# Kernel optimization log

Hardware: AMD Instinct MI355X
Metric: run time of the kernel (lower is better)

The kernel has to match this reference:

```python
import jax, jax.numpy as jnp
import numpy as np

C, CH, H = 128, 32, 4  # c_in, c_hidden, n_head


def _layer_norm(x, w, b, eps=1e-5):
    mu = jnp.mean(x, axis=-1, keepdims=True)
    var = jnp.var(x, axis=-1, keepdims=True)
    return (x - mu) * jax.lax.rsqrt(var + eps) * w + b


def _tri_attn(x, ln_w, ln_b, wq, wk, wv, wz, wg, bg, wo, bo):
    # x: [B, I, J, C]; attention runs over J independently for each row I
    B, I, J, _ = x.shape
    x = _layer_norm(x, ln_w, ln_b)
    q = (x @ wq).reshape(B, I, J, H, CH) * (CH ** -0.5)
    k = (x @ wk).reshape(B, I, J, H, CH)
    v = (x @ wv).reshape(B, I, J, H, CH)
    # learned pairwise triangle bias: [B, I, J, H] -> [B, 1, H, I, J]
    tb = jnp.transpose(x @ wz, (0, 3, 1, 2))[:, None]
    scores = jnp.einsum('biqhd,bikhd->bihqk', q, k) + tb  # [B, I, H, J, J]
    a = jax.nn.softmax(scores, axis=-1)
    o = jnp.einsum('bihqk,bikhd->biqhd', a, v)
    g = jax.nn.sigmoid(x @ wg + bg).reshape(B, I, J, H, CH)
    o = (o * g).reshape(B, I, J, H * CH)
    return o @ wo + bo


def setup_inputs() -> dict:
    key = jax.random.key(0)
    ks = jax.random.split(key, 16)
    B, N = 1, 256
    inp = {'cmap': jax.random.normal(ks[0], (B, C, N, N), jnp.float32)}
    for i, p in enumerate(['s', 'e']):
        kq, kk, kv, kz, kg, ko = jax.random.split(ks[1 + i], 6)
        sd = 0.02
        inp[p + '_ln_w'] = jnp.ones((C,), jnp.float32)
        inp[p + '_ln_b'] = jnp.zeros((C,), jnp.float32)
        inp[p + '_wq'] = jax.random.normal(kq, (C, H * CH), jnp.float32) * sd
        inp[p + '_wk'] = jax.random.normal(kk, (C, H * CH), jnp.float32) * sd
        inp[p + '_wv'] = jax.random.normal(kv, (C, H * CH), jnp.float32) * sd
        inp[p + '_wz'] = jax.random.normal(kz, (C, H), jnp.float32) * sd
        inp[p + '_wg'] = jax.random.normal(kg, (C, H * CH), jnp.float32) * sd
        inp[p + '_bg'] = jnp.ones((H * CH,), jnp.float32)  # gating bias init = 1
        inp[p + '_wo'] = jax.random.normal(ko, (H * CH, C), jnp.float32) * sd
        inp[p + '_bo'] = jnp.zeros((C,), jnp.float32)
    return inp


def reference(cmap,
              s_ln_w, s_ln_b, s_wq, s_wk, s_wv, s_wz, s_wg, s_bg, s_wo, s_bo,
              e_ln_w, e_ln_b, e_wq, e_wk, e_wv, e_wz, e_wg, e_bg, e_wo, e_bo):
    # cmap: [B, C, I, J] -> channels last [B, I, J, C]
    x = jnp.transpose(cmap, (0, 2, 3, 1))
    # triangle attention around starting node (dropout is identity in eval)
    x = x + _tri_attn(x, s_ln_w, s_ln_b, s_wq, s_wk, s_wv, s_wz, s_wg, s_bg, s_wo, s_bo)
    # triangle attention around ending node: transpose I<->J, attend, transpose back
    xt = jnp.swapaxes(x, 1, 2)
    x = x + jnp.swapaxes(
        _tri_attn(xt, e_ln_w, e_ln_b, e_wq, e_wk, e_wv, e_wz, e_wg, e_bg, e_wo, e_bo), 1, 2)
    return jnp.transpose(x, (0, 3, 1, 2))
```

## Files before the change

### kernel.cpp

```cpp
#include <hip/hip_runtime.h>
#include <hip/hip_bf16.h>

#define NNX 256
#define CCX 128
#define HHX 4
#define CHDX 32
#define NIJ (NNX*NNX)

typedef __hip_bfloat16 bf16;
typedef __hip_bfloat162 bf162;
typedef __attribute__((ext_vector_type(8))) short short8v;
typedef __attribute__((ext_vector_type(4))) float float4v;
typedef __attribute__((ext_vector_type(4))) unsigned int uint4v;

__device__ __forceinline__ float4v MFMA(short8v a, short8v b, float4v c){
  return __builtin_amdgcn_mfma_f32_16x16x32_bf16(a, b, c, 0, 0, 0);
}

__device__ __forceinline__ unsigned pk2(float a, float b){
  unsigned short ua = __bfloat16_as_ushort(__float2bfloat16(a));
  unsigned short ub = __bfloat16_as_ushort(__float2bfloat16(b));
  return (unsigned)ua | ((unsigned)ub << 16);
}
__device__ __forceinline__ float ubf(unsigned short u){
  return __bfloat162float(__ushort_as_bfloat16(u));
}

__device__ __forceinline__ void load8bf16(const bf16* p, float* f){
  const bf162* p2 = (const bf162*)p;
  #pragma unroll
  for(int t=0;t<4;++t){ float2 xy = __bfloat1622float2(p2[t]); f[2*t]=xy.x; f[2*t+1]=xy.y; }
}

__global__ __launch_bounds__(256) void k_tin(const float* __restrict__ in, float* __restrict__ out){
  __shared__ float t[32][33];
  const int i = blockIdx.z, jt = blockIdx.x, ct = blockIdx.y;
  const int tx = threadIdx.x, ty = threadIdx.y;
  #pragma unroll
  for(int k=0;k<32;k+=8){
    int c = ct*32 + ty + k;
    t[ty+k][tx] = in[(size_t)c*NIJ + (size_t)i*NNX + jt*32 + tx];
  }
  __syncthreads();
  #pragma unroll
  for(int k=0;k<32;k+=8){
    int j = jt*32 + ty + k;
    out[((size_t)i*NNX + j)*CCX + ct*32 + tx] = t[tx][ty+k];
  }
}

__global__ __launch_bounds__(256) void k_tout(const float* __restrict__ x, float* __restrict__ out){
  __shared__ float t[32][33];
  const int i = blockIdx.z, jt = blockIdx.x, ct = blockIdx.y;
  const int tx = threadIdx.x, ty = threadIdx.y;
  #pragma unroll
  for(int k=0;k<32;k+=8){
    t[ty+k][tx] = x[((size_t)i*NNX + jt*32+ty+k)*CCX + ct*32 + tx];
  }
  __syncthreads();
  #pragma unroll
  for(int k=0;k<32;k+=8){
    out[(size_t)(ct*32+ty+k)*NIJ + (size_t)i*NNX + jt*32 + tx] = t[tx][ty+k];
  }
}

template<int TRANS>
__global__ __launch_bounds__(256) void k_lntb(const float* __restrict__ x,
    const float* __restrict__ w, const float* __restrict__ b,
    const float* __restrict__ wz, bf16* __restrict__ xln, float* __restrict__ tb2){
  const int r = blockIdx.x*4 + threadIdx.y;
  const int ii = r>>8, jj = r&255;
  const float* src = x + (size_t)(TRANS ? (jj*NNX+ii) : r)*CCX;
  const int c = threadIdx.x*2;
  float2 v = *(const float2*)(src+c);
  float s = v.x+v.y, s2 = v.x*v.x+v.y*v.y;
  #pragma unroll
  for(int off=32; off>0; off>>=1){ s += __shfl_xor(s,off); s2 += __shfl_xor(s2,off); }
  float mu = s*0.0078125f;
  float var = s2*0.0078125f - mu*mu;
  float rs = rsqrtf(var+1e-5f);
  float a0 = (v.x-mu)*rs*w[c]+b[c];
  float a1 = (v.y-mu)*rs*w[c+1]+b[c+1];
  bf162 hp; hp.x = __float2bfloat16(a0); hp.y = __float2bfloat16(a1);
  *(bf162*)(xln + (size_t)r*CCX + c) = hp;
  float acc[4];
  #pragma unroll
  for(int hh=0;hh<4;++hh) acc[hh] = a0*wz[c*4+hh] + a1*wz[(c+1)*4+hh];
  #pragma unroll
  for(int off=32; off>0; off>>=1){
    #pragma unroll
    for(int hh=0;hh<4;++hh) acc[hh] += __shfl_xor(acc[hh], off);
  }
  if(threadIdx.x==0){
    #pragma unroll
    for(int hh=0;hh<4;++hh) tb2[(size_t)hh*NIJ + r] = acc[hh];
  }
}

__global__ __launch_bounds__(256) void k_cvtw(const float* __restrict__ wq,
    const float* __restrict__ wk, const float* __restrict__ wv,
    const float* __restrict__ wg, const float* __restrict__ wo, bf16* __restrict__ wT){
  int idx = blockIdx.x*256 + threadIdx.x;
  if(idx < 65536){
    int n = idx >> 7, k = idx & 127;
    const float* W = (n<128)?wq:(n<256)?wk:(n<384)?wv:wg;
    wT[idx] = __float2bfloat16(W[k*CCX + (n&127)]);
  } else {
    int idx2 = idx - 65536;
    int n = idx2 >> 7, k = idx2 & 127;
    wT[idx] = __float2bfloat16(wo[k*CCX + n]);
  }
}

template<int SUB>
__device__ __forceinline__ void attn_sub(const int mb,
    const int lq, const int g, const int l,
    short8v qf, uint2 pgl, uint2 pgh,
    char* ksb, const char* vtb, const float* tbq_base, bf16* __restrict__ obh){
  const int q0 = mb + SUB*16;
  const int q  = q0 + lq;
  const float* tbq = tbq_base + (size_t)q*NNX;
  float4v s[16];
  __builtin_amdgcn_s_setprio(1);
  #pragma unroll
  for(int t=0;t<16;++t){
    short8v ak = *(const short8v*)(ksb + (size_t)(t*16 + lq)*80 + g*16);
    float4v bb = *(const float4v*)(tbq + t*16 + g*4);
    s[t] = MFMA(ak, qf, bb);
  }
  __builtin_amdgcn_s_setprio(0);
  float m = -1e30f;
  #pragma unroll
  for(int t=0;t<16;++t)
    m = fmaxf(m, fmaxf(fmaxf(s[t][0], s[t][1]), fmaxf(s[t][2], s[t][3])));
  m = fmaxf(m, __shfl_xor(m,16));
  m = fmaxf(m, __shfl_xor(m,32));
  float lsum = 0.f;
  #pragma unroll
  for(int t=0;t<16;++t){
    #pragma unroll
    for(int r=0;r<4;++r){ float e = __expf(s[t][r]-m); s[t][r]=e; lsum+=e; }
  }
  lsum += __shfl_xor(lsum,16);
  lsum += __shfl_xor(lsum,32);
  const float linv = 1.0f/lsum;
  #pragma unroll
  for(int dt=0; dt<2; ++dt){
    float4v acc = (float4v)(0.f);
    __builtin_amdgcn_s_setprio(1);
    #pragma unroll
    for(int c=0;c<8;++c){
      const int vrow = dt*16 + lq;
      short8v av = *(const short8v*)(vtb + (size_t)vrow*512 + ((16*g + 64*c) ^ ((vrow&7)<<4)));
      uint4 pb;
      pb.x = pk2(s[2*c][0],   s[2*c][1]);
      pb.y = pk2(s[2*c][2],   s[2*c][3]);
      pb.z = pk2(s[2*c+1][0], s[2*c+1][1]);
      pb.w = pk2(s[2*c+1][2], s[2*c+1][3]);
      short8v bp;
      bp[0]=(short)(pb.x&0xffff); bp[1]=(short)(pb.x>>16);
      bp[2]=(short)(pb.y&0xffff); bp[3]=(short)(pb.y>>16);
      bp[4]=(short)(pb.z&0xffff); bp[5]=(short)(pb.z>>16);
      bp[6]=(short)(pb.w&0xffff); bp[7]=(short)(pb.w>>16);
      acc = MFMA(av, bp, acc);
    }
    __builtin_amdgcn_s_setprio(0);
    const uint2 pg = dt ? pgh : pgl;
    float g0 = ubf((unsigned short)(pg.x & 0xffff));
    float g1 = ubf((unsigned short)(pg.x >> 16));
    float g2 = ubf((unsigned short)(pg.y & 0xffff));
    float g3 = ubf((unsigned short)(pg.y >> 16));
    float o0 = acc[0]*linv / (1.f + __expf(-g0));
    float o1 = acc[1]*linv / (1.f + __expf(-g1));
    float o2 = acc[2]*linv / (1.f + __expf(-g2));
    float o3 = acc[3]*linv / (1.f + __expf(-g3));
    uint2 pw; pw.x = pk2(o0,o1); pw.y = pk2(o2,o3);
    *(uint2*)(ksb + (size_t)(mb + lq*4 + 2*dt + (g>>1))*80 + 64 + (g&1)*8) = pw;
  }
  {
    const int r2 = l >> 2, c2 = l & 3;
    uint4v ow = *(const uint4v*)(ksb + (size_t)(mb + r2*4 + c2)*80 + 64);
    __builtin_nontemporal_store(ow, (uint4v*)(obh + (size_t)(q0 + r2)*CHDX + c2*8));
  }
}

__global__ __launch_bounds__(256,4) void k_fattn(const bf16* __restrict__ xln,
    const bf16* __restrict__ wT, const float* __restrict__ bg,
    const float* __restrict__ tb2, bf16* __restrict__ op){
  __shared__ unsigned short Ks[256*40];
  __shared__ unsigned short Vt[32*256];
  const int id = blockIdx.x;
  const int h = id >> 8, i = id & 255;
  const int tid = threadIdx.x;
  const int w = tid >> 6, l = tid & 63;
  const int lq = l & 15, g = l >> 4;
  const int mb = w*64;

  char* ksb = (char*)Ks;
  char* vtb = (char*)Vt;

  short8v bx[4][4];
  #pragma unroll
  for(int ms=0; ms<4; ++ms){
    const size_t row = (size_t)i*NNX + mb + ms*16 + lq;
    #pragma unroll
    for(int kc=0; kc<4; ++kc)
      bx[ms][kc] = *(const short8v*)(xln + row*CCX + kc*32 + g*8);
  }

  uint4v qfr[4];
  uint2 pgl[4], pgh[4];

  {
    uint2 pqa[4][2];
    #pragma unroll
    for(int half=0; half<2; ++half){
      const int n0 = h*32 + half*16;
      float4v acc[4];
      #pragma unroll
      for(int ms=0; ms<4; ++ms) acc[ms] = (float4v)(0.f);
      #pragma unroll
      for(int kc=0; kc<4; ++kc){
        short8v aw = *(const short8v*)(wT + (size_t)(n0 + lq)*CCX + kc*32 + g*8);
        #pragma unroll
        for(int ms=0; ms<4; ++ms) acc[ms] = MFMA(aw, bx[ms][kc], acc[ms]);
      }
      #pragma unroll
      for(int ms=0; ms<4; ++ms){
        pqa[ms][half].x = pk2(acc[ms][0]*0.17677669529663687f, acc[ms][1]*0.17677669529663687f);
        pqa[ms][half].y = pk2(acc[ms][2]*0.17677669529663687f, acc[ms][3]*0.17677669529663687f);
      }
    }
    const int srcA = lq + 32*(g&1);
    const int hsel = g >> 1;
    #pragma unroll
    for(int ms=0; ms<4; ++ms){
      unsigned sx = hsel ? pqa[ms][1].x : pqa[ms][0].x;
      unsigned sy = hsel ? pqa[ms][1].y : pqa[ms][0].y;
      qfr[ms].x = __shfl(sx, srcA);
      qfr[ms].y = __shfl(sy, srcA);
      qfr[ms].z = __shfl(sx, srcA+16);
      qfr[ms].w = __shfl(sy, srcA+16);
    }
  }

  #pragma unroll
  for(int half=0; half<2; ++half){
    const int n0 = 128 + h*32 + half*16;
    float4v acc[4];
    #pragma unroll
    for(int ms=0; ms<4; ++ms) acc[ms] = (float4v)(0.f);
    #pragma unroll
    for(int kc=0; kc<4; ++kc){
      short8v aw = *(const short8v*)(wT + (size_t)(n0 + lq)*CCX + kc*32 + g*8);
      #pragma unroll
      for(int ms=0; ms<4; ++ms) acc[ms] = MFMA(aw, bx[ms][kc], acc[ms]);
    }
    #pragma unroll
    for(int ms=0; ms<4; ++ms){
      const int row = mb + ms*16 + lq;
      uint2 pw; pw.x = pk2(acc[ms][0], acc[ms][1]);
                pw.y = pk2(acc[ms][2], acc[ms][3]);
      *(uint2*)(ksb + (size_t)row*80 + half*32 + g*8) = pw;
    }
  }

  #pragma unroll
  for(int half=0; half<2; ++half){
    const int n0 = 256 + h*32 + half*16;
    float4v acc[4];
    #pragma unroll
    for(int ms=0; ms<4; ++ms) acc[ms] = (float4v)(0.f);
    #pragma unroll
    for(int kc=0; kc<4; ++kc){
      short8v aw = *(const short8v*)(wT + (size_t)(n0 + lq)*CCX + kc*32 + g*8);
      #pragma unroll
      for(int ms=0; ms<4; ++ms) acc[ms] = MFMA(aw, bx[ms][kc], acc[ms]);
    }
    #pragma unroll
    for(int ms=0; ms<4; ++ms){
      const int k = mb + ms*16 + lq;
      const int j = k & 31;
      const int kap = (k & ~31) + 8*((j>>2)&3) + 4*((j>>4)&1) + (j&3);
      #pragma unroll
      for(int r=0; r<4; ++r){
        const int d = half*16 + 4*g + r;
        const int off = d*512 + ((2*kap) ^ ((d&7)<<4));
        *(unsigned short*)(vtb + off) = __bfloat16_as_ushort(__float2bfloat16(acc[ms][r]));
      }
    }
  }

  #pragma unroll
  for(int half=0; half<2; ++half){
    const int n0 = 384 + h*32 + half*16;
    float4v acc[4];
    #pragma unroll
    for(int ms=0; ms<4; ++ms) acc[ms] = (float4v)(0.f);
    #pragma unroll
    for(int kc=0; kc<4; ++kc){
      short8v aw = *(const short8v*)(wT + (size_t)(n0 + lq)*CCX + kc*32 + g*8);
      #pragma unroll
      for(int ms=0; ms<4; ++ms) acc[ms] = MFMA(aw, bx[ms][kc], acc[ms]);
    }
    const float4 bg4 = *(const float4*)(bg + h*32 + half*16 + 4*g);
    #pragma unroll
    for(int ms=0; ms<4; ++ms){
      uint2 pw; pw.x = pk2(acc[ms][0]+bg4.x, acc[ms][1]+bg4.y);
                pw.y = pk2(acc[ms][2]+bg4.z, acc[ms][3]+bg4.w);
      if(half==0) pgl[ms] = pw; else pgh[ms] = pw;
    }
  }
  __syncthreads();

  bf16* obh = op + ((size_t)h*NIJ + (size_t)i*NNX)*CHDX;
  const float* tbq_base = tb2 + (size_t)h*NIJ;
  attn_sub<0>(mb, lq, g, l, __builtin_bit_cast(short8v, qfr[0]), pgl[0], pgh[0], ksb, vtb, tbq_base, obh);
  attn_sub<1>(mb, lq, g, l, __builtin_bit_cast(short8v, qfr[1]), pgl[1], pgh[1], ksb, vtb, tbq_base, obh);
  attn_sub<2>(mb, lq, g, l, __builtin_bit_cast(short8v, qfr[2]), pgl[2], pgh[2], ksb, vtb, tbq_base, obh);
  attn_sub<3>(mb, lq, g, l, __builtin_bit_cast(short8v, qfr[3]), pgl[3], pgh[3], ksb, vtb, tbq_base, obh);
}

template<int TRANS>
__global__ __launch_bounds__(256) void k_oprojm(const bf16* __restrict__ ob,
    const bf16* __restrict__ woT, const float* __restrict__ bo, float* __restrict__ x){
  const int tid = threadIdx.x;
  const int w = tid >> 6, l = tid & 63;
  const int lq = l & 15, g = l >> 4;
  const int mbase = blockIdx.x*128 + w*32;
  short8v bx[2][4];
  #pragma unroll
  for(int ms=0; ms<2; ++ms){
    const size_t mrow = mbase + ms*16 + lq;
    #pragma unroll
    for(int kc=0; kc<4; ++kc)
      bx[ms][kc] = *(const short8v*)(ob + ((size_t)kc*NIJ + mrow)*CHDX + g*8);
  }
  #pragma unroll
  for(int nj=0; nj<8; ++nj){
    float4v acc0 = (float4v)(0.f), acc1 = (float4v)(0.f);
    #pragma unroll
    for(int kc=0; kc<4; ++kc){
      short8v aw = *(const short8v*)(woT + (size_t)(nj*16 + lq)*CCX + kc*32 + g*8);
      acc0 = MFMA(aw, bx[0][kc], acc0);
      acc1 = MFMA(aw, bx[1][kc], acc1);
    }
    const int col = nj*16 + 4*g;
    const float4 bo4 = *(const float4*)(bo + col);
    #pragma unroll
    for(int ms=0; ms<2; ++ms){
      const int r = mbase + ms*16 + lq;
      const int ii = r>>8, jj = r&255;
      float* dst = x + (size_t)(TRANS ? (jj*NNX+ii) : r)*CCX + col;
      float4 xv = *(float4*)dst;
      xv.x += ((ms==0)?acc0[0]:acc1[0]) + bo4.x;
      xv.y += ((ms==0)?acc0[1]:acc1[1]) + bo4.y;
      xv.z += ((ms==0)?acc0[2]:acc1[2]) + bo4.z;
      xv.w += ((ms==0)?acc0[3]:acc1[3]) + bo4.w;
      *(float4*)dst = xv;
    }
  }
}

extern "C" void kernel_launch(void* const* d_in, const int* in_sizes, int n_in,
                              void* d_out, int out_size, void* d_ws, size_t ws_size,
                              hipStream_t stream){
  const float* cmap = (const float*)d_in[0];
  char* ws = (char*)d_ws;
  float* x   = (float*)(ws);
  bf16* xln  = (bf16*)(ws + 33554432);
  bf16* ob   = (bf16*)(ws + 50331648);
  float* tb2 = (float*)(ws + 117440512);
  bf16* wT   = (bf16*)d_out;
  bf16* woT  = wT + 65536;
  float* outp = (float*)d_out;

  k_tin<<<dim3(8,4,NNX), dim3(32,8), 0, stream>>>(cmap, x);

  for(int p=0;p<2;++p){
    const int b = 1 + 10*p;
    const float* lnw = (const float*)d_in[b+0];
    const float* lnb = (const float*)d_in[b+1];
    const float* wq  = (const float*)d_in[b+2];
    const float* wk  = (const float*)d_in[b+3];
    const float* wv  = (const float*)d_in[b+4];
    const float* wz  = (const float*)d_in[b+5];
    const float* wg  = (const float*)d_in[b+6];
    const float* bg  = (const float*)d_in[b+7];
    const float* wo  = (const float*)d_in[b+8];
    const float* bo  = (const float*)d_in[b+9];

    k_cvtw<<<320, 256, 0, stream>>>(wq, wk, wv, wg, wo, wT);

    if(p==0) k_lntb<0><<<NIJ/4, dim3(64,4), 0, stream>>>(x, lnw, lnb, wz, xln, tb2);
    else     k_lntb<1><<<NIJ/4, dim3(64,4), 0, stream>>>(x, lnw, lnb, wz, xln, tb2);

    k_fattn<<<1024, 256, 0, stream>>>(xln, wT, bg, tb2, ob);

    if(p==0) k_oprojm<0><<<NIJ/128, 256, 0, stream>>>(ob, woT, bo, x);
    else     k_oprojm<1><<<NIJ/128, 256, 0, stream>>>(ob, woT, bo, x);
  }

  k_tout<<<dim3(8,4,NNX), dim3(32,8), 0, stream>>>(x, outp);
}
```

Measured before the change: 250.3 us.

## Fuse input transpose with first layernorm; stage Q in LDS instead of shuffles

Replaces the separate channels-last transpose kernel with a fused kernel that transposes cmap through shared memory and, in the same pass, computes layernorm, the bf16 normalized activations and the triangle bias for the first attention. This drops one full read and write of the activation tensor. In the attention kernel, Q is now written to a new LDS buffer and reloaded per sub-tile rather than redistributed across lanes with shuffles, and the s_setprio hints are removed. The extra LDS lowers the launch-bounds occupancy hint from 4 to 2 blocks, which may reduce latency hiding.

New measurement: 238.2 us. -4.8%, faster.

```diff
diff --git a/kernel.cpp b/kernel.cpp
--- a/kernel.cpp
+++ b/kernel.cpp
@@ -26,29 +26,6 @@
   return __bfloat162float(__ushort_as_bfloat16(u));
 }
 
-__device__ __forceinline__ void load8bf16(const bf16* p, float* f){
-  const bf162* p2 = (const bf162*)p;
-  #pragma unroll
-  for(int t=0;t<4;++t){ float2 xy = __bfloat1622float2(p2[t]); f[2*t]=xy.x; f[2*t+1]=xy.y; }
-}
-
-__global__ __launch_bounds__(256) void k_tin(const float* __restrict__ in, float* __restrict__ out){
-  __shared__ float t[32][33];
-  const int i = blockIdx.z, jt = blockIdx.x, ct = blockIdx.y;
-  const int tx = threadIdx.x, ty = threadIdx.y;
-  #pragma unroll
-  for(int k=0;k<32;k+=8){
-    int c = ct*32 + ty + k;
-    t[ty+k][tx] = in[(size_t)c*NIJ + (size_t)i*NNX + jt*32 + tx];
-  }
-  __syncthreads();
-  #pragma unroll
-  for(int k=0;k<32;k+=8){
-    int j = jt*32 + ty + k;
-    out[((size_t)i*NNX + j)*CCX + ct*32 + tx] = t[tx][ty+k];
-  }
-}
-
 __global__ __launch_bounds__(256) void k_tout(const float* __restrict__ x, float* __restrict__ out){
   __shared__ float t[32][33];
   const int i = blockIdx.z, jt = blockIdx.x, ct = blockIdx.y;
@@ -61,6 +38,66 @@
   #pragma unroll
   for(int k=0;k<32;k+=8){
     out[(size_t)(ct*32+ty+k)*NIJ + (size_t)i*NNX + jt*32 + tx] = t[tx][ty+k];
+  }
+}
+
+__global__ __launch_bounds__(256) void k_lntin(const float* __restrict__ cmap,
+    const float* __restrict__ w, const float* __restrict__ b,
+    const float* __restrict__ wz, float* __restrict__ x,
+    bf16* __restrict__ xln, float* __restrict__ tb2){
+  __shared__ float t[32][130];
+  const int jt = blockIdx.x, i = blockIdx.y;
+  const int tx = threadIdx.x, ty = threadIdx.y;
+  #pragma unroll
+  for(int kk=0; kk<16; ++kk){
+    const int c = kk*8 + ty;
+    t[tx][c] = cmap[(size_t)c*NIJ + (size_t)i*NNX + jt*32 + tx];
+  }
+  __syncthreads();
+  const int tid = ty*32 + tx;
+  const int row = tid >> 3, cs = tid & 7;
+  const int c0 = cs*16;
+  float v[16];
+  #pragma unroll
+  for(int u=0;u<16;++u) v[u] = t[row][c0+u];
+  float s=0.f, s2=0.f;
+  #pragma unroll
+  for(int u=0;u<16;++u){ s += v[u]; s2 += v[u]*v[u]; }
+  #pragma unroll
+  for(int off=4; off>0; off>>=1){ s += __shfl_xor(s,off); s2 += __shfl_xor(s2,off); }
+  const float mu = s*0.0078125f;
+  const float var = s2*0.0078125f - mu*mu;
+  const float rs = rsqrtf(var+1e-5f);
+  const int r = i*NNX + jt*32 + row;
+  float a[16];
+  #pragma unroll
+  for(int u=0;u<16;++u) a[u] = (v[u]-mu)*rs*w[c0+u]+b[c0+u];
+  float* xd = x + (size_t)r*CCX + c0;
+  #pragma unroll
+  for(int u4=0;u4<4;++u4){
+    float4 f4; f4.x=v[u4*4]; f4.y=v[u4*4+1]; f4.z=v[u4*4+2]; f4.w=v[u4*4+3];
+    *(float4*)(xd + u4*4) = f4;
+  }
+  bf16* xl = xln + (size_t)r*CCX + c0;
+  #pragma unroll
+  for(int u8=0;u8<4;++u8){
+    uint2 pw; pw.x = pk2(a[u8*4], a[u8*4+1]); pw.y = pk2(a[u8*4+2], a[u8*4+3]);
+    *(uint2*)(xl + u8*4) = pw;
+  }
+  float acc[4] = {0.f,0.f,0.f,0.f};
+  #pragma unroll
+  for(int u=0;u<16;++u){
+    #pragma unroll
+    for(int hh=0;hh<4;++hh) acc[hh] += a[u]*wz[(c0+u)*4+hh];
+  }
+  #pragma unroll
+  for(int off=4; off>0; off>>=1){
+    #pragma unroll
+    for(int hh=0;hh<4;++hh) acc[hh] += __shfl_xor(acc[hh], off);
+  }
+  if(cs==0){
+    #pragma unroll
+    for(int hh=0;hh<4;++hh) tb2[(size_t)hh*NIJ + r] = acc[hh];
   }
 }
 
@@ -115,20 +152,20 @@
 template<int SUB>
 __device__ __forceinline__ void attn_sub(const int mb,
     const int lq, const int g, const int l,
-    short8v qf, uint2 pgl, uint2 pgh,
-    char* ksb, const char* vtb, const float* tbq_base, bf16* __restrict__ obh){
+    uint2 pgl, uint2 pgh,
+    const char* qsb, char* ksb, const char* vtb,
+    const float* tbq_base, bf16* __restrict__ obh){
   const int q0 = mb + SUB*16;
   const int q  = q0 + lq;
+  short8v qf = *(const short8v*)(qsb + (size_t)q*80 + g*16);
   const float* tbq = tbq_base + (size_t)q*NNX;
   float4v s[16];
-  __builtin_amdgcn_s_setprio(1);
   #pragma unroll
   for(int t=0;t<16;++t){
     short8v ak = *(const short8v*)(ksb + (size_t)(t*16 + lq)*80 + g*16);
     float4v bb = *(const float4v*)(tbq + t*16 + g*4);
     s[t] = MFMA(ak, qf, bb);
   }
-  __builtin_amdgcn_s_setprio(0);
   float m = -1e30f;
   #pragma unroll
   for(int t=0;t<16;++t)
@@ -147,7 +184,6 @@
   #pragma unroll
   for(int dt=0; dt<2; ++dt){
     float4v acc = (float4v)(0.f);
-    __builtin_amdgcn_s_setprio(1);
     #pragma unroll
     for(int c=0;c<8;++c){
       const int vrow = dt*16 + lq;
@@ -164,7 +200,6 @@
       bp[6]=(short)(pb.w&0xffff); bp[7]=(short)(pb.w>>16);
       acc = MFMA(av, bp, acc);
     }
-    __builtin_amdgcn_s_setprio(0);
     const uint2 pg = dt ? pgh : pgl;
     float g0 = ubf((unsigned short)(pg.x & 0xffff));
     float g1 = ubf((unsigned short)(pg.x >> 16));
@@ -184,9 +219,10 @@
   }
 }
 
-__global__ __launch_bounds__(256,4) void k_fattn(const bf16* __restrict__ xln,
+__global__ __launch_bounds__(256,2) void k_fattn(const bf16* __restrict__ xln,
     const bf16* __restrict__ wT, const float* __restrict__ bg,
     const float* __restrict__ tb2, bf16* __restrict__ op){
+  __shared__ unsigned short Qs[256*40];
   __shared__ unsigned short Ks[256*40];
   __shared__ unsigned short Vt[32*256];
   const int id = blockIdx.x;
@@ -196,6 +232,7 @@
   const int lq = l & 15, g = l >> 4;
   const int mb = w*64;
 
+  char* qsb = (char*)Qs;
   char* ksb = (char*)Ks;
   char* vtb = (char*)Vt;
 
@@ -207,43 +244,28 @@
     for(int kc=0; kc<4; ++kc)
       bx[ms][kc] = *(const short8v*)(xln + row*CCX + kc*32 + g*8);
   }
-
-  uint4v qfr[4];
   uint2 pgl[4], pgh[4];
 
-  {
-    uint2 pqa[4][2];
-    #pragma unroll
-    for(int half=0; half<2; ++half){
-      const int n0 = h*32 + half*16;
-      float4v acc[4];
+  #pragma unroll
+  for(int half=0; half<2; ++half){
+    const int n0 = h*32 + half*16;
+    float4v acc[4];
+    #pragma unroll
+    for(int ms=0; ms<4; ++ms) acc[ms] = (float4v)(0.f);
+    #pragma unroll
+    for(int kc=0; kc<4; ++kc){
+      short8v aw = *(const short8v*)(wT + (size_t)(n0 + lq)*CCX + kc*32 + g*8);
       #pragma unroll
-      for(int ms=0; ms<4; ++ms) acc[ms] = (float4v)(0.f);
-      #pragma unroll
-      for(int kc=0; kc<4; ++kc){
-        short8v aw = *(const short8v*)(wT + (size_t)(n0 + lq)*CCX + kc*32 + g*8);
-        #pragma unroll
-        for(int ms=0; ms<4; ++ms) acc[ms] = MFMA(aw, bx[ms][kc], acc[ms]);
-      }
-      #pragma unroll
-      for(int ms=0; ms<4; ++ms){
-        pqa[ms][half].x = pk2(acc[ms][0]*0.17677669529663687f, acc[ms][1]*0.17677669529663687f);
-        pqa[ms][half].y = pk2(acc[ms][2]*0.17677669529663687f, acc[ms][3]*0.17677669529663687f);
-      }
-    }
-    const int srcA = lq + 32*(g&1);
-    const int hsel = g >> 1;
+      for(int ms=0; ms<4; ++ms) acc[ms] = MFMA(aw, bx[ms][kc], acc[ms]);
+    }
     #pragma unroll
     for(int ms=0; ms<4; ++ms){
-      unsigned sx = hsel ? pqa[ms][1].x : pqa[ms][0].x;
-      unsigned sy = hsel ? pqa[ms][1].y : pqa[ms][0].y;
-      qfr[ms].x = __shfl(sx, srcA);
-      qfr[ms].y = __shfl(sy, srcA);
-      qfr[ms].z = __shfl(sx, srcA+16);
-      qfr[ms].w = __shfl(sy, srcA+16);
-    }
-  }
-
+      const int row = mb + ms*16 + lq;
+      uint2 pw; pw.x = pk2(acc[ms][0]*0.17677669529663687f, acc[ms][1]*0.17677669529663687f);
+                pw.y = pk2(acc[ms][2]*0.17677669529663687f, acc[ms][3]*0.17677669529663687f);
+      *(uint2*)(qsb + (size_t)row*80 + half*32 + g*8) = pw;
+    }
+  }
   #pragma unroll
   for(int half=0; half<2; ++half){
     const int n0 = 128 + h*32 + half*16;
@@ -264,7 +286,6 @@
       *(uint2*)(ksb + (size_t)row*80 + half*32 + g*8) = pw;
     }
   }
-
   #pragma unroll
   for(int half=0; half<2; ++half){
     const int n0 = 256 + h*32 + half*16;
@@ -290,7 +311,6 @@
       }
     }
   }
-
   #pragma unroll
   for(int half=0; half<2; ++half){
     const int n0 = 384 + h*32 + half*16;
@@ -315,10 +335,10 @@
 
   bf16* obh = op + ((size_t)h*NIJ + (size_t)i*NNX)*CHDX;
   const float* tbq_base = tb2 + (size_t)h*NIJ;
-  attn_sub<0>(mb, lq, g, l, __builtin_bit_cast(short8v, qfr[0]), pgl[0], pgh[0], ksb, vtb, tbq_base, obh);
-  attn_sub<1>(mb, lq, g, l, __builtin_bit_cast(short8v, qfr[1]), pgl[1], pgh[1], ksb, vtb, tbq_base, obh);
-  attn_sub<2>(mb, lq, g, l, __builtin_bit_cast(short8v, qfr[2]), pgl[2], pgh[2], ksb, vtb, tbq_base, obh);
-  attn_sub<3>(mb, lq, g, l, __builtin_bit_cast(short8v, qfr[3]), pgl[3], pgh[3], ksb, vtb, tbq_base, obh);
+  attn_sub<0>(mb, lq, g, l, pgl[0], pgh[0], qsb, ksb, vtb, tbq_base, obh);
+  attn_sub<1>(mb, lq, g, l, pgl[1], pgh[1], qsb, ksb, vtb, tbq_base, obh);
+  attn_sub<2>(mb, lq, g, l, pgl[2], pgh[2], qsb, ksb, vtb, tbq_base, obh);
+  attn_sub<3>(mb, lq, g, l, pgl[3], pgh[3], qsb, ksb, vtb, tbq_base, obh);
 }
 
 template<int TRANS>
@@ -375,8 +395,6 @@
   bf16* woT  = wT + 65536;
   float* outp = (float*)d_out;
 
-  k_tin<<<dim3(8,4,NNX), dim3(32,8), 0, stream>>>(cmap, x);
-
   for(int p=0;p<2;++p){
     const int b = 1 + 10*p;
     const float* lnw = (const float*)d_in[b+0];
@@ -392,7 +410,7 @@
 
     k_cvtw<<<320, 256, 0, stream>>>(wq, wk, wv, wg, wo, wT);
 
-    if(p==0) k_lntb<0><<<NIJ/4, dim3(64,4), 0, stream>>>(x, lnw, lnb, wz, xln, tb2);
+    if(p==0) k_lntin<<<dim3(8,NNX), dim3(32,8), 0, stream>>>(cmap, lnw, lnb, wz, x, xln, tb2);
     else     k_lntb<1><<<NIJ/4, dim3(64,4), 0, stream>>>(x, lnw, lnb, wz, xln, tb2);
 
     k_fattn<<<1024, 256, 0, stream>>>(xln, wT, bg, tb2, ob);
```
